# Performance work log

Hardware: AMD Instinct MI355X
Metric: run time of the kernel (lower is better)

## Reference

```python
import jax, jax.numpy as jnp
import numpy as np

S, B, V, E, H = 64, 32, 32000, 512, 1024


def gru_cell(x, h, Wih, Whh, bih, bhh):
    # PyTorch GRU cell math. x: [B, in], h: [B, H]
    gi = x @ Wih.T + bih          # [B, 3H]
    gh = h @ Whh.T + bhh          # [B, 3H]
    ir, iz, inn = jnp.split(gi, 3, axis=-1)
    hr, hz, hn = jnp.split(gh, 3, axis=-1)
    r = jax.nn.sigmoid(ir + hr)
    z = jax.nn.sigmoid(iz + hz)
    n = jnp.tanh(inn + r * hn)
    return (1.0 - z) * n + z * h


def run_gru(xs, h0, Wih, Whh, bih, bhh):
    def step(h, x):
        h = gru_cell(x, h, Wih, Whh, bih, bhh)
        return h, h
    _, hs = jax.lax.scan(step, h0, xs)
    return hs  # [S, B, H]


def setup_inputs():
    key = jax.random.key(0)
    ks = jax.random.split(key, 24)
    n = lambda k, shp, s=0.05: (jax.random.normal(k, shp, jnp.float32) * s)
    inp = {
        "input_seq": jax.random.randint(ks[0], (S, B), 0, V),
        "target_seq": jax.random.randint(ks[1], (S, B), 0, V),
        "emb": n(ks[2], (V, E)),
        # bidirectional encoder GRU (forward / backward directions)
        "enc_Wih_f": n(ks[3], (3 * H, E)), "enc_Whh_f": n(ks[4], (3 * H, H)),
        "enc_bih_f": n(ks[5], (3 * H,)),  "enc_bhh_f": n(ks[6], (3 * H,)),
        "enc_Wih_b": n(ks[7], (3 * H, E)), "enc_Whh_b": n(ks[8], (3 * H, H)),
        "enc_bih_b": n(ks[9], (3 * H,)),  "enc_bhh_b": n(ks[10], (3 * H,)),
        "encoder_init": n(ks[11], (2, H), 0.1),
        # decoder GRU: input = token(E) + glimpse(2H) + last_output(E)
        "dec_Wih": n(ks[12], (3 * H, 2 * E + 2 * H)), "dec_Whh": n(ks[13], (3 * H, H)),
        "dec_bih": n(ks[14], (3 * H,)), "dec_bhh": n(ks[15], (3 * H,)),
        "dec_init_h": n(ks[16], (H,), 0.1),
        "dec_init_out": n(ks[17], (E,), 0.1),
        "attn_W1": n(ks[18], (H, 3 * H)),  # Linear(3H -> H, bias=False)
        "attn_W2": n(ks[19], (1, H)),      # Linear(H -> 1, bias=False)
        "out_W": n(ks[20], (V, H)), "out_b": n(ks[21], (V,)),
    }
    return inp


def reference(input_seq, target_seq, emb,
              enc_Wih_f, enc_Whh_f, enc_bih_f, enc_bhh_f,
              enc_Wih_b, enc_Whh_b, enc_bih_b, enc_bhh_b, encoder_init,
              dec_Wih, dec_Whh, dec_bih, dec_bhh, dec_init_h, dec_init_out,
              attn_W1, attn_W2, out_W, out_b):
    x = emb[input_seq]            # [S, B, E]
    tgt = emb[target_seq]         # [S, B, E]
    bsz = x.shape[1]

    # bidirectional encoder
    h0f = jnp.broadcast_to(encoder_init[0], (bsz, H))
    h0b = jnp.broadcast_to(encoder_init[1], (bsz, H))
    fwd = run_gru(x, h0f, enc_Wih_f, enc_Whh_f, enc_bih_f, enc_bhh_f)
    bwd = run_gru(x[::-1], h0b, enc_Wih_b, enc_Whh_b, enc_bih_b, enc_bhh_b)[::-1]
    enc = jnp.concatenate([fwd, bwd], axis=-1)  # [S, B, 2H]

    def step(carry, inp_t):
        h, last_out = carry                      # [B,H], [B,E]
        tok, tg = inp_t                          # [B,E], [B,E]
        hexp = jnp.broadcast_to(h[None], (S, bsz, H))
        a = jnp.concatenate([enc, hexp], axis=-1)            # [S, B, 3H]
        scores = jnp.tanh(a @ attn_W1.T) @ attn_W2.T          # [S, B, 1]
        # NOTE: original uses nn.Softmax(dim=1) on [S,B,1] -> softmax over BATCH dim
        w = jax.nn.softmax(scores, axis=1)
        glimpse = (enc * w).sum(axis=0)                       # [B, 2H]
        dec_in = jnp.concatenate([tok, glimpse, last_out], axis=-1)
        h = gru_cell(dec_in, h, dec_Wih, dec_Whh, dec_bih, dec_bhh)
        probs = jax.nn.softmax(h @ out_W.T + out_b, axis=1)   # [B, V]
        return (h, tg), probs

    h0 = jnp.broadcast_to(dec_init_h, (bsz, H))
    o0 = jnp.broadcast_to(dec_init_out, (bsz, E))
    _, outs = jax.lax.scan(step, (h0, o0), (x, tgt))
    return outs  # [S, B, V]
```

## Files before the change

kernel.cpp:

```cpp
#include <hip/hip_runtime.h>
#include <hip/hip_bf16.h>

#define S_ 64
#define B_ 32
#define V_ 32000
#define E_ 512
#define H_ 1024
#define H3_ 3072

typedef __hip_bfloat16 bf16;
typedef __attribute__((ext_vector_type(8))) short s8v;
typedef __attribute__((ext_vector_type(4))) float f4;
typedef unsigned long long ull;

__device__ __forceinline__ float b2f(bf16 x){ return __bfloat162float(x); }
__device__ __forceinline__ bf16  f2b(float x){ return __float2bfloat16(x); }
__device__ __forceinline__ float bfu2f(unsigned short u){
  union { unsigned u; float f; } c; c.u = ((unsigned)u) << 16; return c.f;
}
#define MFMA16(a,b,c) __builtin_amdgcn_mfma_f32_16x16x32_bf16((a),(b),(c),0,0,0)

__device__ __forceinline__ float fsigmoid(float x){ return 1.f/(1.f + __expf(-x)); }
__device__ __forceinline__ float ftanh(float x){ float e2 = __expf(2.f*x); return 1.f - 2.f/(e2 + 1.f); }

__global__ __launch_bounds__(256) void cast_bf16_k(const float* __restrict__ s, bf16* __restrict__ d, int n8){
  int stride = gridDim.x*256;
  for (int i = blockIdx.x*256 + threadIdx.x; i < n8; i += stride){
    f4 a = *((const f4*)s + (size_t)i*2);
    f4 b = *((const f4*)s + (size_t)i*2 + 1);
    union { s8v v; bf16 h[8]; } o;
    #pragma unroll
    for (int k=0;k<4;k++){ o.h[k]=f2b(a[k]); o.h[4+k]=f2b(b[k]); }
    *((s8v*)d + i) = o.v;
  }
}
__global__ __launch_bounds__(256) void gather_x_k(const float* __restrict__ emb, const int* __restrict__ seq, bf16* __restrict__ d){
  int i = blockIdx.x*256 + threadIdx.x;
  int row = i >> 6, e8 = i & 63;
  const float* src = emb + (size_t)seq[row]*E_;
  f4 a = *((const f4*)src + e8*2);
  f4 b = *((const f4*)src + e8*2 + 1);
  union { s8v v; bf16 h[8]; } o;
  #pragma unroll
  for (int k=0;k<4;k++){ o.h[k]=f2b(a[k]); o.h[4+k]=f2b(b[k]); }
  *((s8v*)d + i) = o.v;
}
__global__ __launch_bounds__(256) void gather_lo_k(const float* __restrict__ emb, const int* __restrict__ tseq, const float* __restrict__ o0, bf16* __restrict__ d){
  int i = blockIdx.x*256 + threadIdx.x;
  int row = i >> 6, e8 = i & 63;
  int t = row >> 5, b = row & 31;
  const float* src = (t == 0) ? o0 : (emb + (size_t)tseq[(t-1)*B_ + b]*E_);
  f4 a = *((const f4*)src + e8*2);
  f4 c = *((const f4*)src + e8*2 + 1);
  union { s8v v; bf16 h[8]; } o;
  #pragma unroll
  for (int k=0;k<4;k++){ o.h[k]=f2b(a[k]); o.h[4+k]=f2b(c[k]); }
  *((s8v*)d + i) = o.v;
}

template<int WB16, int ACC>
__global__ __launch_bounds__(256) void gemm_bt(const bf16* __restrict__ A, int lda,
                                               const bf16* __restrict__ B, int ldb,
                                               const float* __restrict__ bias,
                                               void* __restrict__ Cp, int ldc, int K)
{
  __shared__ bf16 a_sm[128][40];
  __shared__ bf16 b_sm[128][40];
  const int tid = threadIdx.x;
  const int m0 = blockIdx.y*128, n0 = blockIdx.x*128;
  const int w = tid>>6, l = tid&63;
  const int wm = w>>1, wn = w&1;
  f4 acc[4][4];
  #pragma unroll
  for (int i=0;i<4;i++)
    #pragma unroll
    for (int j=0;j<4;j++) acc[i][j] = (f4){0.f,0.f,0.f,0.f};
  const int srow = tid>>1, skc = (tid&1)*16;
  const int ar = l&15, koff = (l>>4)*8;
  for (int k0 = 0; k0 < K; k0 += 32){
    __syncthreads();
    const s8v* pa = (const s8v*)(A + (size_t)(m0+srow)*lda + k0 + skc);
    const s8v* pb = (const s8v*)(B + (size_t)(n0+srow)*ldb + k0 + skc);
    *(s8v*)&a_sm[srow][skc]   = pa[0];
    *(s8v*)&a_sm[srow][skc+8] = pa[1];
    *(s8v*)&b_sm[srow][skc]   = pb[0];
    *(s8v*)&b_sm[srow][skc+8] = pb[1];
    __syncthreads();
    s8v av[4], bv[4];
    #pragma unroll
    for (int i=0;i<4;i++) av[i] = *(const s8v*)&a_sm[wm*64 + i*16 + ar][koff];
    #pragma unroll
    for (int j=0;j<4;j++) bv[j] = *(const s8v*)&b_sm[wn*64 + j*16 + ar][koff];
    #pragma unroll
    for (int i=0;i<4;i++)
      #pragma unroll
      for (int j=0;j<4;j++)
        acc[i][j] = MFMA16(av[i], bv[j], acc[i][j]);
  }
  const int rb = (l>>4)*4;
  #pragma unroll
  for (int i=0;i<4;i++){
    #pragma unroll
    for (int j=0;j<4;j++){
      int col = n0 + wn*64 + j*16 + ar;
      float badd = bias ? bias[col] : 0.f;
      #pragma unroll
      for (int r=0;r<4;r++){
        int row = m0 + wm*64 + i*16 + rb + r;
        size_t idx = (size_t)row*ldc + col;
        float v = acc[i][j][r] + badd;
        if (ACC) v += ((const float*)Cp)[idx];
        if (WB16) ((bf16*)Cp)[idx] = f2b(v);
        else      ((float*)Cp)[idx] = v;
      }
    }
  }
}

__global__ __launch_bounds__(256) void enc_init_k(const float* __restrict__ enc_init,
                                                  bf16* __restrict__ hb0, float* __restrict__ hfE){
  int i = blockIdx.x*256 + threadIdx.x;
  int base = i*8;
  int dir = base>>15, rem = base&32767, col = rem&1023;
  const float* sp = enc_init + dir*H_ + col;
  f4 a = *(const f4*)sp, b = *(const f4*)(sp+4);
  union { s8v v; bf16 h[8]; } o;
  #pragma unroll
  for (int k=0;k<4;k++){ o.h[k]=f2b(a[k]); o.h[4+k]=f2b(b[k]); }
  *(s8v*)(hb0 + dir*32768 + rem) = o.v;
  *(f4*)(hfE + dir*32768 + rem) = a;
  *(f4*)(hfE + dir*32768 + rem + 4) = b;
}
__global__ __launch_bounds__(256) void dec_init_k(const float* __restrict__ dinh,
                                                  bf16* __restrict__ hd0, float* __restrict__ hfD){
  int i = blockIdx.x*256 + threadIdx.x;
  int base = i*8;
  int col = base&1023;
  const float* sp = dinh + col;
  f4 a = *(const f4*)sp, b = *(const f4*)(sp+4);
  union { s8v v; bf16 h[8]; } o;
  #pragma unroll
  for (int k=0;k<4;k++){ o.h[k]=f2b(a[k]); o.h[4+k]=f2b(b[k]); }
  *(s8v*)(hd0 + base) = o.v;
  *(f4*)(hfD + base) = a;
  *(f4*)(hfD + base + 4) = b;
}

__global__ __launch_bounds__(256) void enc_step_k(
  const float* __restrict__ gi_f, const float* __restrict__ gi_b,
  const bf16* __restrict__ whhf, const bf16* __restrict__ whhb,
  const float* __restrict__ bhhf, const float* __restrict__ bhhb,
  const bf16* __restrict__ hrd_base,
  bf16* __restrict__ hwr_base,
  float* __restrict__ hfE,
  bf16* __restrict__ enc_out, int s)
{
  __shared__ bf16 hst[16][1032];
  __shared__ bf16 hsT[16][64];
  const int tid = threadIdx.x, bid = blockIdx.x;
  const int w = tid>>6, l = tid&63;
  const int lr = l&15, koff = (l>>4)*8, rb = (l>>4)*4;
  const int x = bid&7, g3 = bid>>3;
  const int dir = x>>2;
  const int mt = g3>>2;
  const int jtb = (x&3)*16 + (g3&3)*4;
  const int jt = jtb + w;
  const int col = jt*16 + lr;
  const bf16* W    = dir ? whhb : whhf;
  const float* gi  = dir ? gi_b : gi_f;
  const float* bhh = dir ? bhhb : bhhf;
  const float br_ = bhh[col], bz_ = bhh[H_+col], bn_ = bhh[2*H_+col];
  const bf16* pr = W + (size_t)(jt*16 + lr)*H_ + koff;
  const bf16* pz = pr + (size_t)H_*H_;
  const bf16* pn = pz + (size_t)H_*H_;
  {
    const bf16* src = hrd_base + dir*32768 + (size_t)mt*16*H_;
    #pragma unroll
    for (int c = 0; c < 8; ++c){
      int g = c*256 + tid;
      int row = g>>7, off = g&127;
      *(s8v*)&hst[row][off*8] = *(const s8v*)(src + (size_t)row*H_ + off*8);
    }
  }
  __syncthreads();
  f4 accr = (f4){0,0,0,0}, accz = (f4){0,0,0,0}, accn = (f4){0,0,0,0};
  #pragma unroll 4
  for (int k0 = 0; k0 < H_; k0 += 32){
    s8v a = *(const s8v*)&hst[lr][koff + k0];
    accr = MFMA16(a, *(const s8v*)(pr + k0), accr);
    accz = MFMA16(a, *(const s8v*)(pz + k0), accz);
    accn = MFMA16(a, *(const s8v*)(pn + k0), accn);
  }
  const int es = dir ? (63 - s) : s;
  #pragma unroll
  for (int ri = 0; ri < 4; ++ri){
    const int b_ = mt*16 + rb + ri;
    const size_t gr = (size_t)(es*B_ + b_)*H3_;
    float ir = gi[gr + col], iz = gi[gr + H_ + col], inn = gi[gr + 2*H_ + col];
    float rg = fsigmoid(ir + accr[ri] + br_);
    float zg = fsigmoid(iz + accz[ri] + bz_);
    float ng = ftanh(inn + rg*(accn[ri] + bn_));
    float hold = hfE[dir*32768 + b_*H_ + col];
    float hnew = (1.f - zg)*ng + zg*hold;
    hfE[dir*32768 + b_*H_ + col] = hnew;
    hsT[rb+ri][w*16+lr] = f2b(hnew);
  }
  __syncthreads();
  {
    const int row = tid>>4, seg = tid&15;
    ull v = *(ull*)&hsT[row][seg*4];
    *(ull*)(hwr_base + dir*32768 + (size_t)(mt*16+row)*H_ + jtb*16 + seg*4) = v;
    *(ull*)(enc_out + (size_t)(es*B_ + mt*16+row)*2048 + dir*H_ + jtb*16 + seg*4) = v;
  }
}

__global__ __launch_bounds__(256) void dec_k1(
  const bf16* __restrict__ hd,
  const bf16* __restrict__ whhd, const float* __restrict__ bhhd,
  const bf16* __restrict__ w1b,
  float* __restrict__ gh, bf16* __restrict__ hW1b)
{
  __shared__ bf16 hst[16][1032];
  __shared__ float ghT[16][128];
  __shared__ bf16 hwT[16][128];
  const int tid = threadIdx.x, bid = blockIdx.x;
  const int w = tid>>6, l = tid&63;
  const int lr = l&15, koff = (l>>4)*8;
  const bool isP = bid < 16;
  const int hmt = isP ? (bid&1) : ((bid-16)&1);
  {
    const bf16* src = hd + (size_t)hmt*16*H_;
    #pragma unroll
    for (int c = 0; c < 8; ++c){
      int g = c*256 + tid;
      int row = g>>7, off = g&127;
      *(s8v*)&hst[row][off*8] = *(const s8v*)(src + (size_t)row*H_ + off*8);
    }
  }
  __syncthreads();
  if (isP){
    const int x2 = bid>>1;
    const int pjt0 = x2*8 + w*2;
    #pragma unroll
    for (int q = 0; q < 2; ++q){
      const bf16* pb = w1b + (size_t)((pjt0+q)*16 + lr)*H3_ + 2048 + koff;
      f4 acc = (f4){0,0,0,0};
      #pragma unroll 4
      for (int k0 = 0; k0 < H_; k0 += 32)
        acc = MFMA16(*(const s8v*)&hst[lr][koff+k0], *(const s8v*)(pb+k0), acc);
      #pragma unroll
      for (int r = 0; r < 4; ++r)
        hwT[(l>>4)*4+r][(w*2+q)*16 + lr] = f2b(acc[r]);
    }
    __syncthreads();
    #pragma unroll
    for (int i = 0; i < 2; ++i){
      int idx = tid + i*256;
      int row = idx>>5, seg = idx&31;
      *(ull*)(hW1b + (size_t)(hmt*16+row)*H_ + x2*128 + seg*4) = *(ull*)&hwT[row][seg*4];
    }
  } else {
    const int gb = bid - 16;
    const int rest = gb>>1;
    const int x3 = rest/3, gkk = rest%3;
    const int ntb = x3*24 + gkk*8;
    #pragma unroll
    for (int q = 0; q < 2; ++q){
      const int nt = ntb + w*2 + q;
      const bf16* pb = whhd + (size_t)(nt*16 + lr)*H_ + koff;
      const float bv = bhhd[nt*16 + lr];
      f4 acc = (f4){0,0,0,0};
      #pragma unroll 4
      for (int k0 = 0; k0 < H_; k0 += 32)
        acc = MFMA16(*(const s8v*)&hst[lr][koff+k0], *(const s8v*)(pb+k0), acc);
      #pragma unroll
      for (int r = 0; r < 4; ++r)
        ghT[(l>>4)*4+r][(w*2+q)*16 + lr] = acc[r] + bv;
    }
    __syncthreads();
    #pragma unroll
    for (int i = 0; i < 4; ++i){
      int idx = tid + i*256;
      int row = idx>>6, seg = idx&63;
      union{ float f[2]; ull u; } pk;
      pk.f[0] = ghT[row][seg*2]; pk.f[1] = ghT[row][seg*2+1];
      *(ull*)(gh + (size_t)(hmt*16+row)*H3_ + ntb*16 + seg*2) = pk.u;
    }
  }
}

__global__ __launch_bounds__(256) void dec_k2(
  const bf16* __restrict__ encW1b, const bf16* __restrict__ hW1b,
  const float* __restrict__ attnW2, float* __restrict__ wat)
{
  __shared__ float w2st[1024];
  __shared__ float scl[32];
  const int tid = threadIdx.x, s = blockIdx.x;
  w2st[tid] = attnW2[tid];
  w2st[tid+256] = attnW2[tid+256];
  w2st[tid+512] = attnW2[tid+512];
  w2st[tid+768] = attnW2[tid+768];
  __syncthreads();
  const int b = tid>>3, part = tid&7;
  const bf16* hp = hW1b + (size_t)b*H_ + part*128;
  const bf16* ep = encW1b + ((size_t)s*B_ + b)*H_ + part*128;
  const float* wp = w2st + part*128;
  float p = 0.f;
  #pragma unroll 4
  for (int ii = 0; ii < 16; ++ii){
    union { s8v v; unsigned short uu[8]; } hv, ev;
    hv.v = *(const s8v*)(hp + ii*8);
    ev.v = *(const s8v*)(ep + ii*8);
    #pragma unroll
    for (int k = 0; k < 8; ++k){
      float xx = bfu2f(ev.uu[k]) + bfu2f(hv.uu[k]);
      p += wp[ii*8+k]*ftanh(xx);
    }
  }
  p += __shfl_xor(p,1); p += __shfl_xor(p,2); p += __shfl_xor(p,4);
  if (part == 0) scl[b] = p;
  __syncthreads();
  if (tid < 32){
    float v = scl[tid];
    float m = v;
    #pragma unroll
    for (int o = 1; o <= 16; o <<= 1) m = fmaxf(m, __shfl_xor(m, o));
    float e = __expf(v - m);
    float Z = e;
    #pragma unroll
    for (int o = 1; o <= 16; o <<= 1) Z += __shfl_xor(Z, o);
    wat[s*B_ + tid] = e/Z;
  }
}

__global__ __launch_bounds__(256) void dec_k3(
  const float* __restrict__ gi_t,
  const bf16* __restrict__ encWgb, const float* __restrict__ gh,
  const float* __restrict__ wat,
  float* __restrict__ hfD, bf16* __restrict__ hd_w, bf16* __restrict__ hall_t)
{
  __shared__ float watst[64];
  __shared__ float part_[4][3][256];
  __shared__ bf16 hnewst[256];
  const int tid = threadIdx.x, bid = blockIdx.x;
  const int x = bid&7, g3 = bid>>3;
  const int db = 4*x + (g3&3), jq = g3>>2;
  const int jD = jq*256 + tid;
  if (tid < 64) watst[tid] = wat[tid*B_ + db];
  __syncthreads();
  const int lane = tid&63, wv = tid>>6;
  const int j0 = jq*256 + lane*4;
  f4 g0 = (f4){0,0,0,0}, g1 = (f4){0,0,0,0}, g2 = (f4){0,0,0,0};
  #pragma unroll 4
  for (int i = 0; i < 16; ++i){
    const int s2 = wv*16 + i;
    const float wt = watst[s2];
    const bf16* ro = encWgb + ((size_t)s2*B_ + db)*H3_;
    union{ ull u; unsigned short us[4]; } v0, v1, v2;
    v0.u = *(const ull*)(ro + j0);
    v1.u = *(const ull*)(ro + H_ + j0);
    v2.u = *(const ull*)(ro + 2*H_ + j0);
    #pragma unroll
    for (int k = 0; k < 4; ++k){
      g0[k] += wt*bfu2f(v0.us[k]);
      g1[k] += wt*bfu2f(v1.us[k]);
      g2[k] += wt*bfu2f(v2.us[k]);
    }
  }
  *(f4*)&part_[wv][0][lane*4] = g0;
  *(f4*)&part_[wv][1][lane*4] = g1;
  *(f4*)&part_[wv][2][lane*4] = g2;
  __syncthreads();
  float G0 = part_[0][0][tid]+part_[1][0][tid]+part_[2][0][tid]+part_[3][0][tid];
  float G1 = part_[0][1][tid]+part_[1][1][tid]+part_[2][1][tid]+part_[3][1][tid];
  float G2 = part_[0][2][tid]+part_[1][2][tid]+part_[2][2][tid]+part_[3][2][tid];
  const float* gp = gi_t + (size_t)db*H3_ + jD;
  float ir  = gp[0]    + G0;
  float iz  = gp[H_]   + G1;
  float inn = gp[2*H_] + G2;
  float hr_ = gh[(size_t)db*H3_ + jD];
  float hz_ = gh[(size_t)db*H3_ + H_ + jD];
  float hn_ = gh[(size_t)db*H3_ + 2*H_ + jD];
  float rg = fsigmoid(ir + hr_);
  float zg = fsigmoid(iz + hz_);
  float ng = ftanh(inn + rg*hn_);
  float hold = hfD[(size_t)db*H_ + jD];
  float hnew = (1.f - zg)*ng + zg*hold;
  hfD[(size_t)db*H_ + jD] = hnew;
  hnewst[tid] = f2b(hnew);
  __syncthreads();
  if (tid < 64){
    ull v = *(ull*)&hnewst[tid*4];
    *(ull*)(hd_w + (size_t)db*H_ + jq*256 + tid*4) = v;
    *(ull*)(hall_t + (size_t)db*H_ + jq*256 + tid*4) = v;
  }
}

__global__ __launch_bounds__(256) void softmax_rows_k(float* __restrict__ out){
  __shared__ float wm[4], wl[4];
  const int tid = threadIdx.x;
  float* p = out + (size_t)blockIdx.x*V_;
  float m = -1e30f, lsum = 0.f;
  for (int j = tid; j < V_; j += 256){
    float v = p[j];
    float mn = fmaxf(m, v);
    lsum = lsum*__expf(m - mn) + __expf(v - mn);
    m = mn;
  }
  #pragma unroll
  for (int o = 32; o; o >>= 1){
    float mo = __shfl_xor(m, o), lo_ = __shfl_xor(lsum, o);
    float mn = fmaxf(m, mo);
    lsum = lsum*__expf(m - mn) + lo_*__expf(mo - mn);
    m = mn;
  }
  if ((tid&63)==0){ wm[tid>>6] = m; wl[tid>>6] = lsum; }
  __syncthreads();
  float M = fmaxf(fmaxf(wm[0],wm[1]), fmaxf(wm[2],wm[3]));
  float L = wl[0]*__expf(wm[0]-M) + wl[1]*__expf(wm[1]-M)
          + wl[2]*__expf(wm[2]-M) + wl[3]*__expf(wm[3]-M);
  float inv = 1.f/L;
  for (int j = tid; j < V_; j += 256) p[j] = __expf(p[j]-M)*inv;
}

extern "C" void kernel_launch(void* const* d_in, const int* in_sizes, int n_in,
                              void* d_out, int out_size, void* d_ws, size_t ws_size,
                              hipStream_t stream)
{
  (void)in_sizes; (void)n_in; (void)out_size; (void)ws_size;
  const int*   iseq  = (const int*)d_in[0];
  const int*   tseq  = (const int*)d_in[1];
  const float* emb   = (const float*)d_in[2];
  const float* wihf  = (const float*)d_in[3];
  const float* whhf_f= (const float*)d_in[4];
  const float* bihf  = (const float*)d_in[5];
  const float* bhhf  = (const float*)d_in[6];
  const float* wihb  = (const float*)d_in[7];
  const float* whhb_f= (const float*)d_in[8];
  const float* bihb  = (const float*)d_in[9];
  const float* bhhb  = (const float*)d_in[10];
  const float* einit = (const float*)d_in[11];
  const float* wihd  = (const float*)d_in[12];
  const float* whhd_f= (const float*)d_in[13];
  const float* bihd  = (const float*)d_in[14];
  const float* bhhd  = (const float*)d_in[15];
  const float* dinh  = (const float*)d_in[16];
  const float* dino  = (const float*)d_in[17];
  const float* w1    = (const float*)d_in[18];
  const float* w2    = (const float*)d_in[19];
  const float* outw  = (const float*)d_in[20];
  const float* outb  = (const float*)d_in[21];
  float* out = (float*)d_out;

  char* ws = (char*)d_ws;
  size_t off = 0;
  auto alloc = [&](size_t bytes)->char*{ char* p = ws + off; off += (bytes + 255) & ~(size_t)255; return p; };
  bf16* x_b      = (bf16*)alloc((size_t)2048*512*2);
  bf16* lo_b     = (bf16*)alloc((size_t)2048*512*2);
  bf16* wihf_b   = (bf16*)alloc((size_t)3072*512*2);
  bf16* wihb_b   = (bf16*)alloc((size_t)3072*512*2);
  bf16* whhf_b   = (bf16*)alloc((size_t)3072*1024*2);
  bf16* whhb_b   = (bf16*)alloc((size_t)3072*1024*2);
  bf16* wihd_b   = (bf16*)alloc((size_t)3072*3072*2);
  bf16* whhd_b   = (bf16*)alloc((size_t)3072*1024*2);
  bf16* w1_b     = (bf16*)alloc((size_t)1024*3072*2);
  bf16* outw_b   = (bf16*)alloc((size_t)32000*1024*2);
  float* gi_f    = (float*)alloc((size_t)2048*3072*4);
  float* gi_b    = (float*)alloc((size_t)2048*3072*4);
  float* gi_d    = (float*)alloc((size_t)2048*3072*4);
  bf16* enc_b    = (bf16*)alloc((size_t)2048*2048*2);
  bf16* encW1_b  = (bf16*)alloc((size_t)2048*1024*2);
  bf16* encWg_b  = (bf16*)alloc((size_t)2048*3072*2);
  bf16*  henc_b  = (bf16*)alloc((size_t)2*65536*2);
  float* hfE     = (float*)alloc((size_t)2*32768*4);
  bf16*  hdb     = (bf16*)alloc((size_t)2*32768*2);
  float* hfD     = (float*)alloc((size_t)32768*4);
  bf16*  hW1b    = (bf16*)alloc((size_t)32768*2);
  float* ghb     = (float*)alloc((size_t)32*3072*4);
  float* wat     = (float*)alloc((size_t)64*32*4);
  bf16*  hall_b  = (bf16*)alloc((size_t)2048*1024*2);

  auto cgrid = [](int n8){ int g = (n8 + 255)/256; return g > 2048 ? 2048 : g; };
  gather_x_k <<<512, 256, 0, stream>>>(emb, iseq, x_b);
  gather_lo_k<<<512, 256, 0, stream>>>(emb, tseq, dino, lo_b);
  cast_bf16_k<<<cgrid(196608),  256, 0, stream>>>(wihf,   wihf_b, 196608);
  cast_bf16_k<<<cgrid(196608),  256, 0, stream>>>(wihb,   wihb_b, 196608);
  cast_bf16_k<<<cgrid(393216),  256, 0, stream>>>(whhf_f, whhf_b, 393216);
  cast_bf16_k<<<cgrid(393216),  256, 0, stream>>>(whhb_f, whhb_b, 393216);
  cast_bf16_k<<<cgrid(1179648), 256, 0, stream>>>(wihd,   wihd_b, 1179648);
  cast_bf16_k<<<cgrid(393216),  256, 0, stream>>>(whhd_f, whhd_b, 393216);
  cast_bf16_k<<<cgrid(393216),  256, 0, stream>>>(w1,     w1_b,   393216);
  cast_bf16_k<<<cgrid(4096000), 256, 0, stream>>>(outw,   outw_b, 4096000);

  gemm_bt<0,0><<<dim3(24,16), 256, 0, stream>>>(x_b, 512, wihf_b,      512,  bihf,    gi_f, 3072, 512);
  gemm_bt<0,0><<<dim3(24,16), 256, 0, stream>>>(x_b, 512, wihb_b,      512,  bihb,    gi_b, 3072, 512);
  gemm_bt<0,0><<<dim3(24,16), 256, 0, stream>>>(x_b, 512, wihd_b,      3072, bihd,    gi_d, 3072, 512);
  gemm_bt<0,1><<<dim3(24,16), 256, 0, stream>>>(lo_b,512, wihd_b+2560, 3072, nullptr, gi_d, 3072, 512);

  enc_init_k<<<32, 256, 0, stream>>>(einit, henc_b, hfE);
  for (int s = 0; s < 64; ++s){
    const bf16* hrd = henc_b + (size_t)(s&1)*65536;
    bf16*       hwr = henc_b + (size_t)((s+1)&1)*65536;
    enc_step_k<<<64, 256, 0, stream>>>(gi_f, gi_b, whhf_b, whhb_b, bhhf, bhhb,
                                       hrd, hwr, hfE, enc_b, s);
  }

  gemm_bt<1,0><<<dim3(8,16),  256, 0, stream>>>(enc_b, 2048, w1_b,       3072, nullptr, encW1_b, 1024, 2048);
  gemm_bt<1,0><<<dim3(24,16), 256, 0, stream>>>(enc_b, 2048, wihd_b+512, 3072, nullptr, encWg_b, 3072, 2048);

  dec_init_k<<<16, 256, 0, stream>>>(dinh, hdb, hfD);
  for (int t = 0; t < 64; ++t){
    const bf16* hdr = hdb + (size_t)(t&1)*32768;
    bf16*       hdw = hdb + (size_t)((t+1)&1)*32768;
    dec_k1<<<64, 256, 0, stream>>>(hdr, whhd_b, bhhd, w1_b, ghb, hW1b);
    dec_k2<<<64, 256, 0, stream>>>(encW1_b, hW1b, w2, wat);
    dec_k3<<<128, 256, 0, stream>>>(gi_d + (size_t)t*B_*H3_, encWg_b, ghb, wat,
                                    hfD, hdw, hall_b + (size_t)t*B_*H_);
  }

  gemm_bt<0,0><<<dim3(250,16), 256, 0, stream>>>(hall_b, 1024, outw_b, 1024, outb, out, 32000, 1024);
  softmax_rows_k<<<2048, 256, 0, stream>>>(out);
}
```

Measured before the change: 3.279 ms.

## Store logits in bf16, swizzle output GEMM, merge casts, gathers and encoder projections

The output projection now writes bf16 logits into a scratch region through a new GEMM with an XCD-aware tile ordering. Softmax is split into a stats pass and a normalize pass that reads the bf16 logits and writes fp32 probabilities, cutting the fp32 round-trip traffic of the old in-place softmax. Separately, several cast and gather launches are merged into multi-tensor kernels. The forward and backward encoder input projections become one GEMM over the contiguous weight pair with a concatenated bias. Rounding logits to bf16 before softmax adds a small precision loss, and the scratch logits alias the start of the workspace, so buffer placement matters.

```diff
diff --git a/kernel.cpp b/kernel.cpp
--- a/kernel.cpp
+++ b/kernel.cpp
@@ -34,27 +34,57 @@
     *((s8v*)d + i) = o.v;
   }
 }
-__global__ __launch_bounds__(256) void gather_x_k(const float* __restrict__ emb, const int* __restrict__ seq, bf16* __restrict__ d){
+__global__ __launch_bounds__(256) void cast2_k(const float* __restrict__ s0, const float* __restrict__ s1,
+                                               bf16* __restrict__ d0, bf16* __restrict__ d1, int n8){
+  const float* s = blockIdx.y ? s1 : s0;
+  bf16* d = blockIdx.y ? d1 : d0;
+  int stride = gridDim.x*256;
+  for (int i = blockIdx.x*256 + threadIdx.x; i < n8; i += stride){
+    f4 a = *((const f4*)s + (size_t)i*2);
+    f4 b = *((const f4*)s + (size_t)i*2 + 1);
+    union { s8v v; bf16 h[8]; } o;
+    #pragma unroll
+    for (int k=0;k<4;k++){ o.h[k]=f2b(a[k]); o.h[4+k]=f2b(b[k]); }
+    *((s8v*)d + i) = o.v;
+  }
+}
+__global__ __launch_bounds__(256) void cast4_k(const float* __restrict__ s0, const float* __restrict__ s1,
+                                               const float* __restrict__ s2, const float* __restrict__ s3,
+                                               bf16* __restrict__ d0, bf16* __restrict__ d1,
+                                               bf16* __restrict__ d2, bf16* __restrict__ d3, int n8){
+  const float* s = (blockIdx.y==0)?s0:(blockIdx.y==1)?s1:(blockIdx.y==2)?s2:s3;
+  bf16* d = (blockIdx.y==0)?d0:(blockIdx.y==1)?d1:(blockIdx.y==2)?d2:d3;
+  int stride = gridDim.x*256;
+  for (int i = blockIdx.x*256 + threadIdx.x; i < n8; i += stride){
+    f4 a = *((const f4*)s + (size_t)i*2);
+    f4 b = *((const f4*)s + (size_t)i*2 + 1);
+    union { s8v v; bf16 h[8]; } o;
+    #pragma unroll
+    for (int k=0;k<4;k++){ o.h[k]=f2b(a[k]); o.h[4+k]=f2b(b[k]); }
+    *((s8v*)d + i) = o.v;
+  }
+}
+__global__ __launch_bounds__(256) void gather2_k(const float* __restrict__ emb,
+                                                 const int* __restrict__ iseq, const int* __restrict__ tseq,
+                                                 const float* __restrict__ o0,
+                                                 bf16* __restrict__ dx, bf16* __restrict__ dlo){
   int i = blockIdx.x*256 + threadIdx.x;
   int row = i >> 6, e8 = i & 63;
-  const float* src = emb + (size_t)seq[row]*E_;
+  const float* src;
+  bf16* d;
+  if (blockIdx.y == 0){
+    src = emb + (size_t)iseq[row]*E_;
+    d = dx;
+  } else {
+    int t = row >> 5, b = row & 31;
+    src = (t == 0) ? o0 : (emb + (size_t)tseq[(t-1)*B_ + b]*E_);
+    d = dlo;
+  }
   f4 a = *((const f4*)src + e8*2);
   f4 b = *((const f4*)src + e8*2 + 1);
   union { s8v v; bf16 h[8]; } o;
   #pragma unroll
   for (int k=0;k<4;k++){ o.h[k]=f2b(a[k]); o.h[4+k]=f2b(b[k]); }
-  *((s8v*)d + i) = o.v;
-}
-__global__ __launch_bounds__(256) void gather_lo_k(const float* __restrict__ emb, const int* __restrict__ tseq, const float* __restrict__ o0, bf16* __restrict__ d){
-  int i = blockIdx.x*256 + threadIdx.x;
-  int row = i >> 6, e8 = i & 63;
-  int t = row >> 5, b = row & 31;
-  const float* src = (t == 0) ? o0 : (emb + (size_t)tseq[(t-1)*B_ + b]*E_);
-  f4 a = *((const f4*)src + e8*2);
-  f4 c = *((const f4*)src + e8*2 + 1);
-  union { s8v v; bf16 h[8]; } o;
-  #pragma unroll
-  for (int k=0;k<4;k++){ o.h[k]=f2b(a[k]); o.h[4+k]=f2b(c[k]); }
   *((s8v*)d + i) = o.v;
 }
 
@@ -117,8 +147,129 @@
   }
 }
 
+__global__ __launch_bounds__(256) void out_gemm_k(
+  const bf16* __restrict__ A, const bf16* __restrict__ Bw,
+  const float* __restrict__ bias, bf16* __restrict__ C)
+{
+  __shared__ bf16 a_sm[128][40];
+  __shared__ bf16 b_sm[128][40];
+  const int tid = threadIdx.x;
+  const int bid = blockIdx.x;
+  const int xcd = bid & 7, kk = bid >> 3;
+  const int super = kk >> 6, rem = kk & 63;
+  const int sm = super & 1, sn = super >> 1;
+  const int mi = rem & 7, nj = rem >> 3;
+  const int mt = sm*8 + mi, nl = sn*8 + nj;
+  const int nt = nl*8 + xcd;
+  if (nt >= 250) return;
+  const int m0 = mt*128, n0 = nt*128;
+  const int w = tid>>6, l = tid&63;
+  const int wm = w>>1, wn = w&1;
+  f4 acc[4][4];
+  #pragma unroll
+  for (int i=0;i<4;i++)
+    #pragma unroll
+    for (int j=0;j<4;j++) acc[i][j] = (f4){0.f,0.f,0.f,0.f};
+  const int srow = tid>>1, skc = (tid&1)*16;
+  const int ar = l&15, koff = (l>>4)*8;
+  for (int k0 = 0; k0 < 1024; k0 += 32){
+    __syncthreads();
+    const s8v* pa = (const s8v*)(A + (size_t)(m0+srow)*1024 + k0 + skc);
+    const s8v* pb = (const s8v*)(Bw + (size_t)(n0+srow)*1024 + k0 + skc);
+    *(s8v*)&a_sm[srow][skc]   = pa[0];
+    *(s8v*)&a_sm[srow][skc+8] = pa[1];
+    *(s8v*)&b_sm[srow][skc]   = pb[0];
+    *(s8v*)&b_sm[srow][skc+8] = pb[1];
+    __syncthreads();
+    s8v av[4], bv[4];
+    #pragma unroll
+    for (int i=0;i<4;i++) av[i] = *(const s8v*)&a_sm[wm*64 + i*16 + ar][koff];
+    #pragma unroll
+    for (int j=0;j<4;j++) bv[j] = *(const s8v*)&b_sm[wn*64 + j*16 + ar][koff];
+    #pragma unroll
+    for (int i=0;i<4;i++)
+      #pragma unroll
+      for (int j=0;j<4;j++)
+        acc[i][j] = MFMA16(av[i], bv[j], acc[i][j]);
+  }
+  const int rb = (l>>4)*4;
+  float bj[4];
+  #pragma unroll
+  for (int j=0;j<4;j++) bj[j] = bias[n0 + wn*64 + j*16 + ar];
+  #pragma unroll
+  for (int i=0;i<4;i++){
+    #pragma unroll
+    for (int j=0;j<4;j++){
+      const int col = n0 + wn*64 + j*16 + ar;
+      #pragma unroll
+      for (int r=0;r<4;r++){
+        const int row = m0 + wm*64 + i*16 + rb + r;
+        C[(size_t)row*V_ + col] = f2b(acc[i][j][r] + bj[j]);
+      }
+    }
+  }
+}
+
+__global__ __launch_bounds__(256) void logit_stats_k(const bf16* __restrict__ lg,
+                                                     float* __restrict__ rowM, float* __restrict__ rowL){
+  __shared__ float wm[4], wl[4];
+  const int tid = threadIdx.x;
+  const bf16* p = lg + (size_t)blockIdx.x*V_;
+  float m = -1e30f, lsum = 0.f;
+  for (int c = tid; c < V_/8; c += 256){
+    union { s8v v; unsigned short us[8]; } u;
+    u.v = *((const s8v*)p + c);
+    #pragma unroll
+    for (int k = 0; k < 8; ++k){
+      float v = bfu2f(u.us[k]);
+      float mn = fmaxf(m, v);
+      lsum = lsum*__expf(m - mn) + __expf(v - mn);
+      m = mn;
+    }
+  }
+  #pragma unroll
+  for (int o = 32; o; o >>= 1){
+    float mo = __shfl_xor(m, o), lo_ = __shfl_xor(lsum, o);
+    float mn = fmaxf(m, mo);
+    lsum = lsum*__expf(m - mn) + lo_*__expf(mo - mn);
+    m = mn;
+  }
+  if ((tid&63)==0){ wm[tid>>6] = m; wl[tid>>6] = lsum; }
+  __syncthreads();
+  if (tid == 0){
+    float M = fmaxf(fmaxf(wm[0],wm[1]), fmaxf(wm[2],wm[3]));
+    float L = wl[0]*__expf(wm[0]-M) + wl[1]*__expf(wm[1]-M)
+            + wl[2]*__expf(wm[2]-M) + wl[3]*__expf(wm[3]-M);
+    rowM[blockIdx.x] = M;
+    rowL[blockIdx.x] = L;
+  }
+}
+
+__global__ __launch_bounds__(256) void norm_k(const bf16* __restrict__ lg,
+                                              const float* __restrict__ rowM, const float* __restrict__ rowL,
+                                              float* __restrict__ out){
+  const int tid = threadIdx.x;
+  const int row = blockIdx.x;
+  const float M = rowM[row], inv = 1.f/rowL[row];
+  const bf16* p = lg + (size_t)row*V_;
+  float* q = out + (size_t)row*V_;
+  for (int c = tid; c < V_/8; c += 256){
+    union { s8v v; unsigned short us[8]; } u;
+    u.v = *((const s8v*)p + c);
+    f4 o0, o1;
+    #pragma unroll
+    for (int k = 0; k < 4; ++k) o0[k] = __expf(bfu2f(u.us[k]) - M)*inv;
+    #pragma unroll
+    for (int k = 0; k < 4; ++k) o1[k] = __expf(bfu2f(u.us[4+k]) - M)*inv;
+    *((f4*)q + c*2)     = o0;
+    *((f4*)q + c*2 + 1) = o1;
+  }
+}
+
 __global__ __launch_bounds__(256) void enc_init_k(const float* __restrict__ enc_init,
-                                                  bf16* __restrict__ hb0, float* __restrict__ hfE){
+                                                  const float* __restrict__ bihf, const float* __restrict__ bihb,
+                                                  bf16* __restrict__ hb0, float* __restrict__ hfE,
+                                                  float* __restrict__ bias_fb){
   int i = blockIdx.x*256 + threadIdx.x;
   int base = i*8;
   int dir = base>>15, rem = base&32767, col = rem&1023;
@@ -130,6 +281,7 @@
   *(s8v*)(hb0 + dir*32768 + rem) = o.v;
   *(f4*)(hfE + dir*32768 + rem) = a;
   *(f4*)(hfE + dir*32768 + rem + 4) = b;
+  if (i < 6144) bias_fb[i] = (i < 3072) ? bihf[i] : bihb[i-3072];
 }
 __global__ __launch_bounds__(256) void dec_init_k(const float* __restrict__ dinh,
                                                   bf16* __restrict__ hd0, float* __restrict__ hfD){
@@ -147,13 +299,11 @@
 }
 
 __global__ __launch_bounds__(256) void enc_step_k(
-  const float* __restrict__ gi_f, const float* __restrict__ gi_b,
+  const float* __restrict__ gi_fb,
   const bf16* __restrict__ whhf, const bf16* __restrict__ whhb,
   const float* __restrict__ bhhf, const float* __restrict__ bhhb,
-  const bf16* __restrict__ hrd_base,
-  bf16* __restrict__ hwr_base,
-  float* __restrict__ hfE,
-  bf16* __restrict__ enc_out, int s)
+  const bf16* __restrict__ hrd_base, bf16* __restrict__ hwr_base,
+  float* __restrict__ hfE, bf16* __restrict__ enc_out, int s)
 {
   __shared__ bf16 hst[16][1032];
   __shared__ bf16 hsT[16][64];
@@ -167,7 +317,6 @@
   const int jt = jtb + w;
   const int col = jt*16 + lr;
   const bf16* W    = dir ? whhb : whhf;
-  const float* gi  = dir ? gi_b : gi_f;
   const float* bhh = dir ? bhhb : bhhf;
   const float br_ = bhh[col], bz_ = bhh[H_+col], bn_ = bhh[2*H_+col];
   const bf16* pr = W + (size_t)(jt*16 + lr)*H_ + koff;
@@ -192,11 +341,12 @@
     accn = MFMA16(a, *(const s8v*)(pn + k0), accn);
   }
   const int es = dir ? (63 - s) : s;
+  const int dcol = dir*3072 + col;
   #pragma unroll
   for (int ri = 0; ri < 4; ++ri){
     const int b_ = mt*16 + rb + ri;
-    const size_t gr = (size_t)(es*B_ + b_)*H3_;
-    float ir = gi[gr + col], iz = gi[gr + H_ + col], inn = gi[gr + 2*H_ + col];
+    const size_t gr = (size_t)(es*B_ + b_)*6144;
+    float ir = gi_fb[gr + dcol], iz = gi_fb[gr + 1024 + dcol], inn = gi_fb[gr + 2048 + dcol];
     float rg = fsigmoid(ir + accr[ri] + br_);
     float zg = fsigmoid(iz + accz[ri] + bz_);
     float ng = ftanh(inn + rg*(accn[ri] + bn_));
@@ -394,33 +544,6 @@
     *(ull*)(hd_w + (size_t)db*H_ + jq*256 + tid*4) = v;
     *(ull*)(hall_t + (size_t)db*H_ + jq*256 + tid*4) = v;
   }
-}
-
-__global__ __launch_bounds__(256) void softmax_rows_k(float* __restrict__ out){
-  __shared__ float wm[4], wl[4];
-  const int tid = threadIdx.x;
-  float* p = out + (size_t)blockIdx.x*V_;
-  float m = -1e30f, lsum = 0.f;
-  for (int j = tid; j < V_; j += 256){
-    float v = p[j];
-    float mn = fmaxf(m, v);
-    lsum = lsum*__expf(m - mn) + __expf(v - mn);
-    m = mn;
-  }
-  #pragma unroll
-  for (int o = 32; o; o >>= 1){
-    float mo = __shfl_xor(m, o), lo_ = __shfl_xor(lsum, o);
-    float mn = fmaxf(m, mo);
-    lsum = lsum*__expf(m - mn) + lo_*__expf(mo - mn);
-    m = mn;
-  }
-  if ((tid&63)==0){ wm[tid>>6] = m; wl[tid>>6] = lsum; }
-  __syncthreads();
-  float M = fmaxf(fmaxf(wm[0],wm[1]), fmaxf(wm[2],wm[3]));
-  float L = wl[0]*__expf(wm[0]-M) + wl[1]*__expf(wm[1]-M)
-          + wl[2]*__expf(wm[2]-M) + wl[3]*__expf(wm[3]-M);
-  float inv = 1.f/L;
-  for (int j = tid; j < V_; j += 256) p[j] = __expf(p[j]-M)*inv;
 }
 
 extern "C" void kernel_launch(void* const* d_in, const int* in_sizes, int n_in,
@@ -455,6 +578,7 @@
   char* ws = (char*)d_ws;
   size_t off = 0;
   auto alloc = [&](size_t bytes)->char*{ char* p = ws + off; off += (bytes + 255) & ~(size_t)255; return p; };
+  bf16* logits_b = (bf16*)ws;
   bf16* x_b      = (bf16*)alloc((size_t)2048*512*2);
   bf16* lo_b     = (bf16*)alloc((size_t)2048*512*2);
   bf16* wihf_b   = (bf16*)alloc((size_t)3072*512*2);
@@ -464,13 +588,12 @@
   bf16* wihd_b   = (bf16*)alloc((size_t)3072*3072*2);
   bf16* whhd_b   = (bf16*)alloc((size_t)3072*1024*2);
   bf16* w1_b     = (bf16*)alloc((size_t)1024*3072*2);
-  bf16* outw_b   = (bf16*)alloc((size_t)32000*1024*2);
-  float* gi_f    = (float*)alloc((size_t)2048*3072*4);
-  float* gi_b    = (float*)alloc((size_t)2048*3072*4);
+  float* gi_fb   = (float*)alloc((size_t)2048*6144*4);
   float* gi_d    = (float*)alloc((size_t)2048*3072*4);
   bf16* enc_b    = (bf16*)alloc((size_t)2048*2048*2);
   bf16* encW1_b  = (bf16*)alloc((size_t)2048*1024*2);
   bf16* encWg_b  = (bf16*)alloc((size_t)2048*3072*2);
+  float* bias_fb = (float*)alloc((size_t)6144*4);
   bf16*  henc_b  = (bf16*)alloc((size_t)2*65536*2);
   float* hfE     = (float*)alloc((size_t)2*32768*4);
   bf16*  hdb     = (bf16*)alloc((size_t)2*32768*2);
@@ -478,30 +601,27 @@
   bf16*  hW1b    = (bf16*)alloc((size_t)32768*2);
   float* ghb     = (float*)alloc((size_t)32*3072*4);
   float* wat     = (float*)alloc((size_t)64*32*4);
+  float* rowM    = (float*)alloc((size_t)2048*4);
+  float* rowL    = (float*)alloc((size_t)2048*4);
+  bf16* outw_b   = (bf16*)alloc((size_t)32000*1024*2);
   bf16*  hall_b  = (bf16*)alloc((size_t)2048*1024*2);
 
-  auto cgrid = [](int n8){ int g = (n8 + 255)/256; return g > 2048 ? 2048 : g; };
-  gather_x_k <<<512, 256, 0, stream>>>(emb, iseq, x_b);
-  gather_lo_k<<<512, 256, 0, stream>>>(emb, tseq, dino, lo_b);
-  cast_bf16_k<<<cgrid(196608),  256, 0, stream>>>(wihf,   wihf_b, 196608);
-  cast_bf16_k<<<cgrid(196608),  256, 0, stream>>>(wihb,   wihb_b, 196608);
-  cast_bf16_k<<<cgrid(393216),  256, 0, stream>>>(whhf_f, whhf_b, 393216);
-  cast_bf16_k<<<cgrid(393216),  256, 0, stream>>>(whhb_f, whhb_b, 393216);
-  cast_bf16_k<<<cgrid(1179648), 256, 0, stream>>>(wihd,   wihd_b, 1179648);
-  cast_bf16_k<<<cgrid(393216),  256, 0, stream>>>(whhd_f, whhd_b, 393216);
-  cast_bf16_k<<<cgrid(393216),  256, 0, stream>>>(w1,     w1_b,   393216);
-  cast_bf16_k<<<cgrid(4096000), 256, 0, stream>>>(outw,   outw_b, 4096000);
-
-  gemm_bt<0,0><<<dim3(24,16), 256, 0, stream>>>(x_b, 512, wihf_b,      512,  bihf,    gi_f, 3072, 512);
-  gemm_bt<0,0><<<dim3(24,16), 256, 0, stream>>>(x_b, 512, wihb_b,      512,  bihb,    gi_b, 3072, 512);
-  gemm_bt<0,0><<<dim3(24,16), 256, 0, stream>>>(x_b, 512, wihd_b,      3072, bihd,    gi_d, 3072, 512);
-  gemm_bt<0,1><<<dim3(24,16), 256, 0, stream>>>(lo_b,512, wihd_b+2560, 3072, nullptr, gi_d, 3072, 512);
-
-  enc_init_k<<<32, 256, 0, stream>>>(einit, henc_b, hfE);
+  gather2_k<<<dim3(512,2), 256, 0, stream>>>(emb, iseq, tseq, dino, x_b, lo_b);
+  cast2_k<<<dim3(768,2),  256, 0, stream>>>(wihf, wihb, wihf_b, wihb_b, 196608);
+  cast4_k<<<dim3(768,4),  256, 0, stream>>>(whhf_f, whhb_f, whhd_f, w1,
+                                            whhf_b, whhb_b, whhd_b, w1_b, 393216);
+  cast_bf16_k<<<2048, 256, 0, stream>>>(wihd, wihd_b, 1179648);
+  cast_bf16_k<<<2048, 256, 0, stream>>>(outw, outw_b, 4096000);
+  enc_init_k<<<32, 256, 0, stream>>>(einit, bihf, bihb, henc_b, hfE, bias_fb);
+
+  gemm_bt<0,0><<<dim3(48,16), 256, 0, stream>>>(x_b, 512, wihf_b,      512,  bias_fb, gi_fb, 6144, 512);
+  gemm_bt<0,0><<<dim3(24,16), 256, 0, stream>>>(x_b, 512, wihd_b,      3072, bihd,    gi_d,  3072, 512);
+  gemm_bt<0,1><<<dim3(24,16), 256, 0, stream>>>(lo_b,512, wihd_b+2560, 3072, nullptr, gi_d,  3072, 512);
+
   for (int s = 0; s < 64; ++s){
     const bf16* hrd = henc_b + (size_t)(s&1)*65536;
     bf16*       hwr = henc_b + (size_t)((s+1)&1)*65536;
-    enc_step_k<<<64, 256, 0, stream>>>(gi_f, gi_b, whhf_b, whhb_b, bhhf, bhhb,
+    enc_step_k<<<64, 256, 0, stream>>>(gi_fb, whhf_b, whhb_b, bhhf, bhhb,
                                        hrd, hwr, hfE, enc_b, s);
   }
 
@@ -518,6 +638,7 @@
                                     hfD, hdw, hall_b + (size_t)t*B_*H_);
   }
 
-  gemm_bt<0,0><<<dim3(250,16), 256, 0, stream>>>(hall_b, 1024, outw_b, 1024, outb, out, 32000, 1024);
-  softmax_rows_k<<<2048, 256, 0, stream>>>(out);
-}
+  out_gemm_k<<<4096, 256, 0, stream>>>(hall_b, outw_b, outb, logits_b);
+  logit_stats_k<<<2048, 256, 0, stream>>>(logits_b, rowM, rowL);
+  norm_k<<<2048, 256, 0, stream>>>(logits_b, rowM, rowL, out);
+}
```

Measured after the change: 3.162 ms. 3.6% less time.
